# Performance work log

Measured on AMD Instinct MI355X. Metric: run time of the kernel, lower is better.

## Reference

```python
import jax, jax.numpy as jnp
import numpy as np

LEN_SORT_WINDOW = 2


def _butterfly_indices(v_len, d_v):
    # Column j is arange rolled right by s_j: s_0 = s_1 = 0, s_j = 2*(j-1) mod v_len.
    # (The butterfly_factor_to_matrix result in the original code is discarded;
    #  only the cyclic shifts matter.)
    shifts = np.zeros(d_v, dtype=np.int64)
    if d_v > 1:
        shifts[1:] = (LEN_SORT_WINDOW * np.arange(d_v - 1, dtype=np.int64)) % v_len
    rows = np.arange(v_len, dtype=np.int64)[:, None]
    return jnp.asarray((rows - shifts[None, :]) % v_len)  # [v_len, d_v] int64


def setup_inputs() -> dict:
    key = jax.random.key(0)
    B, L, D = 8, 4096, 1024
    v = jax.random.normal(key, (B, L, D), dtype=jnp.float32)
    return {"v": v}


def reference(v) -> jnp.ndarray:
    B, L, D = v.shape
    idx = _butterfly_indices(L, D)                       # [L, D]
    # gather: v_shifted[b,i,j] = v[b, idx[i,j], j]
    v_shifted = jnp.take_along_axis(v, jnp.broadcast_to(idx[None], (B, L, D)), axis=1)
    # windowed pairwise sort (ascending, window = 2) along the sequence dim
    pairs = v_shifted.reshape(B, L // LEN_SORT_WINDOW, LEN_SORT_WINDOW, D)
    v_sorted = jnp.sort(pairs, axis=2)
    return v_sorted.reshape(B, L, D)
```

## Files before the change

kernel.cpp:

```cpp
#include <hip/hip_runtime.h>

namespace {

constexpr int B  = 8;
constexpr int L  = 4096;
constexpr int D  = 1024;
constexpr int D4 = D / 4;
constexpr int P  = L / 2;
constexpr int TJ = 32;
constexpr int G  = TJ / 4;
constexpr int TP = 128;
constexpr int RTOT = TP + TJ;
constexpr int LDW  = TJ + 4;
constexpr int NT = 512;

__global__ __launch_bounds__(NT)
void swd_kernel(const float4* __restrict__ v, float4* __restrict__ out) {
  const int j0 = blockIdx.x * TJ;
  const int p0 = blockIdx.y * TP;
  const int b  = blockIdx.z;

  __shared__ __align__(16) float lds_m[RTOT][LDW];
  __shared__ __align__(16) float lds_M[RTOT][LDW];

  const int hmax = j0 + TJ - 2;
  const int r0   = p0 - hmax;

  const float4* __restrict__ vb = v + (size_t)b * L * D4 + (j0 >> 2);

  for (int idx = threadIdx.x; idx < RTOT * G; idx += NT) {
    const int k  = idx >> 3;
    const int fg = idx & 7;
    const int q  = (r0 + k) & (P - 1);
    const float4 a0 = vb[(size_t)(2 * q) * D4 + fg];
    const float4 a1 = vb[(size_t)(2 * q + 1) * D4 + fg];
    float4 m, M;
    m.x = fminf(a0.x, a1.x); M.x = fmaxf(a0.x, a1.x);
    m.y = fminf(a0.y, a1.y); M.y = fmaxf(a0.y, a1.y);
    m.z = fminf(a0.z, a1.z); M.z = fmaxf(a0.z, a1.z);
    m.w = fminf(a0.w, a1.w); M.w = fmaxf(a0.w, a1.w);
    *(float4*)&lds_m[k][4 * fg] = m;
    *(float4*)&lds_M[k][4 * fg] = M;
  }
  __syncthreads();

  const int g   = threadIdx.x & 7;
  const int c   = threadIdx.x >> 3;
  const int pp0 = c * 2;
  const int kx = pp0 + (TJ - 1) - 4 * g;

  const float4 m0 = *(const float4*)&lds_m[kx - 3][4 * g];
  const float4 m1 = *(const float4*)&lds_m[kx - 2][4 * g];
  const float4 m2 = *(const float4*)&lds_m[kx - 1][4 * g];
  const float4 m3 = *(const float4*)&lds_m[kx    ][4 * g];
  const float4 m4 = *(const float4*)&lds_m[kx + 1][4 * g];
  const float4 M0 = *(const float4*)&lds_M[kx - 3][4 * g];
  const float4 M1 = *(const float4*)&lds_M[kx - 2][4 * g];
  const float4 M2 = *(const float4*)&lds_M[kx - 1][4 * g];
  const float4 M3 = *(const float4*)&lds_M[kx    ][4 * g];
  const float4 M4 = *(const float4*)&lds_M[kx + 1][4 * g];

  const bool sp = (j0 == 0) && (g == 0);

  float4 e0, o0, e1, o1;
  e0.x = sp ? m2.x : m3.x; e0.y = m2.y; e0.z = m1.z; e0.w = m0.w;
  o0.x = sp ? M2.x : M3.x; o0.y = M2.y; o0.z = M1.z; o0.w = M0.w;
  e1.x = sp ? m3.x : m4.x; e1.y = m3.y; e1.z = m2.z; e1.w = m1.w;
  o1.x = sp ? M3.x : M4.x; o1.y = M3.y; o1.z = M2.z; o1.w = M1.w;

  float4* __restrict__ ob = out + (size_t)b * L * D4 + (j0 >> 2) + g;
  const size_t ro = (size_t)(2 * (p0 + pp0)) * D4;
  ob[ro]            = e0;
  ob[ro + D4]       = o0;
  ob[ro + 2 * D4]   = e1;
  ob[ro + 3 * D4]   = o1;
}

}

extern "C" void kernel_launch(void* const* d_in, const int* , int ,
                              void* d_out, int , void* , size_t ,
                              hipStream_t stream) {
  const float4* v = (const float4*)d_in[0];
  float4* out = (float4*)d_out;
  dim3 grid(D / TJ, P / TP, B);
  swd_kernel<<<grid, NT, 0, stream>>>(v, out);
}
```

Measured before the change: 235.8 us.

## Double-buffer async global-to-LDS loads across multiple pair tiles per block

Each block now handles four consecutive pair tiles of 64 instead of one tile of 128. Raw rows are loaded straight into a double-buffered LDS array with global_load_lds, and loading the next tile overlaps with computing the current one, using manual vmcnt waits and barriers. The min/max sort moves from the load phase to the read-from-LDS phase, and launch bounds request higher occupancy. In exchange, the halo overhead per tile grows because the tile is smaller, each pair is recomputed on read, and the hand-written waitcnt logic is fragile.

```diff
diff --git a/kernel.cpp b/kernel.cpp
--- a/kernel.cpp
+++ b/kernel.cpp
@@ -8,72 +8,99 @@
 constexpr int D4 = D / 4;
 constexpr int P  = L / 2;
 constexpr int TJ = 32;
-constexpr int G  = TJ / 4;
-constexpr int TP = 128;
-constexpr int RTOT = TP + TJ;
-constexpr int LDW  = TJ + 4;
+constexpr int TP = 64;
+constexpr int RP = TP + TJ;
+constexpr int RR = 2 * RP;
 constexpr int NT = 512;
+constexpr int NW = NT / 64;
+constexpr int T  = 4;
+constexpr int NCH = RR * TJ * 4 / 1024;
+constexpr int CPW = NCH / NW;
+static_assert(CPW == 3, "vmcnt literal below assumes 3 in-flight chunk loads");
+static_assert(2 * RR * TJ * 4 <= 49152, "LDS must stay well under 64 KiB");
 
-__global__ __launch_bounds__(NT)
-void swd_kernel(const float4* __restrict__ v, float4* __restrict__ out) {
+__device__ __forceinline__ void async_ld16(const float* g, float* l) {
+  __builtin_amdgcn_global_load_lds(
+      (const __attribute__((address_space(1))) void*)g,
+      (__attribute__((address_space(3))) void*)l, 16, 0, 0);
+}
+
+__global__ __launch_bounds__(NT, 6)
+void swd_kernel(const float* __restrict__ v, float4* __restrict__ out) {
   const int j0 = blockIdx.x * TJ;
-  const int p0 = blockIdx.y * TP;
+  const int ty = blockIdx.y;
   const int b  = blockIdx.z;
 
-  __shared__ __align__(16) float lds_m[RTOT][LDW];
-  __shared__ __align__(16) float lds_M[RTOT][LDW];
+  __shared__ float lds[2][RR * TJ];
 
-  const int hmax = j0 + TJ - 2;
-  const int r0   = p0 - hmax;
+  const int tid  = threadIdx.x;
+  const int wave = tid >> 6;
+  const int lane = tid & 63;
 
-  const float4* __restrict__ vb = v + (size_t)b * L * D4 + (j0 >> 2);
+  const float* __restrict__ vb = v + (size_t)b * L * D + j0;
 
-  for (int idx = threadIdx.x; idx < RTOT * G; idx += NT) {
-    const int k  = idx >> 3;
-    const int fg = idx & 7;
-    const int q  = (r0 + k) & (P - 1);
-    const float4 a0 = vb[(size_t)(2 * q) * D4 + fg];
-    const float4 a1 = vb[(size_t)(2 * q + 1) * D4 + fg];
-    float4 m, M;
-    m.x = fminf(a0.x, a1.x); M.x = fmaxf(a0.x, a1.x);
-    m.y = fminf(a0.y, a1.y); M.y = fmaxf(a0.y, a1.y);
-    m.z = fminf(a0.z, a1.z); M.z = fmaxf(a0.z, a1.z);
-    m.w = fminf(a0.w, a1.w); M.w = fmaxf(a0.w, a1.w);
-    *(float4*)&lds_m[k][4 * fg] = m;
-    *(float4*)&lds_M[k][4 * fg] = M;
-  }
-  __syncthreads();
+  const int f  = lane & 7;
+  const int kb = wave * 8 + (lane >> 3);
 
-  const int g   = threadIdx.x & 7;
-  const int c   = threadIdx.x >> 3;
-  const int pp0 = c * 2;
-  const int kx = pp0 + (TJ - 1) - 4 * g;
-
-  const float4 m0 = *(const float4*)&lds_m[kx - 3][4 * g];
-  const float4 m1 = *(const float4*)&lds_m[kx - 2][4 * g];
-  const float4 m2 = *(const float4*)&lds_m[kx - 1][4 * g];
-  const float4 m3 = *(const float4*)&lds_m[kx    ][4 * g];
-  const float4 m4 = *(const float4*)&lds_m[kx + 1][4 * g];
-  const float4 M0 = *(const float4*)&lds_M[kx - 3][4 * g];
-  const float4 M1 = *(const float4*)&lds_M[kx - 2][4 * g];
-  const float4 M2 = *(const float4*)&lds_M[kx - 1][4 * g];
-  const float4 M3 = *(const float4*)&lds_M[kx    ][4 * g];
-  const float4 M4 = *(const float4*)&lds_M[kx + 1][4 * g];
-
+  const int g   = tid & 7;
+  const int c   = tid >> 3;
+  const int krb = 2 * c - 8 * g + 2 * (TJ - 1) - 6;
   const bool sp = (j0 == 0) && (g == 0);
 
-  float4 e0, o0, e1, o1;
-  e0.x = sp ? m2.x : m3.x; e0.y = m2.y; e0.z = m1.z; e0.w = m0.w;
-  o0.x = sp ? M2.x : M3.x; o0.y = M2.y; o0.z = M1.z; o0.w = M0.w;
-  e1.x = sp ? m3.x : m4.x; e1.y = m3.y; e1.z = m2.z; e1.w = m1.w;
-  o1.x = sp ? M3.x : M4.x; o1.y = M3.y; o1.z = M2.z; o1.w = M1.w;
+  float4* __restrict__ ob = out + (size_t)b * L * D4 + (j0 >> 2) + g;
 
-  float4* __restrict__ ob = out + (size_t)b * L * D4 + (j0 >> 2) + g;
-  const size_t ro = (size_t)(2 * (p0 + pp0)) * D4;
-  ob[ro]            = e0;
-  ob[ro + D4]       = o0;
-  ob[ro + 2 * D4]   = e1;
-  ob[ro + 3 * D4]   = o1;
+  auto stage = [&](int tt, int s) {
+    const int p0 = tt * TP;
+    const int r0 = p0 - (j0 + TJ - 2);
+#pragma unroll
+    for (int i = 0; i < CPW; ++i) {
+      const int kr  = kb + 64 * i;
+      const int q   = (r0 + (kr >> 1)) & (P - 1);
+      const int row = 2 * q + (kr & 1);
+      async_ld16(vb + (size_t)row * D + 4 * f,
+                 &lds[s][(wave + NW * i) * (8 * TJ)]);
+    }
+  };
+
+  const int tt0 = ty * T;
+  stage(tt0, 0);
+
+#pragma unroll
+  for (int t = 0; t < T; ++t) {
+    if (t + 1 < T) {
+      stage(tt0 + t + 1, (t + 1) & 1);
+      asm volatile("s_waitcnt vmcnt(3)" ::: "memory");
+    } else {
+      asm volatile("s_waitcnt vmcnt(0)" ::: "memory");
+    }
+    __builtin_amdgcn_s_barrier();
+    asm volatile("" ::: "memory");
+
+    const float* Lb = lds[t & 1];
+
+    float4 m[4], M[4];
+#pragma unroll
+    for (int u = 0; u < 4; ++u) {
+      const float4 a0 = *(const float4*)&Lb[(krb + 2 * u)     * TJ + 4 * g];
+      const float4 a1 = *(const float4*)&Lb[(krb + 2 * u + 1) * TJ + 4 * g];
+      m[u].x = fminf(a0.x, a1.x); M[u].x = fmaxf(a0.x, a1.x);
+      m[u].y = fminf(a0.y, a1.y); M[u].y = fmaxf(a0.y, a1.y);
+      m[u].z = fminf(a0.z, a1.z); M[u].z = fmaxf(a0.z, a1.z);
+      m[u].w = fminf(a0.w, a1.w); M[u].w = fmaxf(a0.w, a1.w);
+    }
+
+    float4 e, o;
+    e.x = sp ? m[2].x : m[3].x; e.y = m[2].y; e.z = m[1].z; e.w = m[0].w;
+    o.x = sp ? M[2].x : M[3].x; o.y = M[2].y; o.z = M[1].z; o.w = M[0].w;
+
+    const size_t ro = (size_t)(2 * ((tt0 + t) * TP + c)) * D4;
+    ob[ro]      = e;
+    ob[ro + D4] = o;
+
+    asm volatile("s_waitcnt lgkmcnt(0)" ::: "memory");
+    __builtin_amdgcn_s_barrier();
+    asm volatile("" ::: "memory");
+  }
 }
 
 }
@@ -81,8 +108,8 @@
 extern "C" void kernel_launch(void* const* d_in, const int* , int ,
                               void* d_out, int , void* , size_t ,
                               hipStream_t stream) {
-  const float4* v = (const float4*)d_in[0];
+  const float* v = (const float*)d_in[0];
   float4* out = (float4*)d_out;
-  dim3 grid(D / TJ, P / TP, B);
+  dim3 grid(D / TJ, P / (T * TP), B);
   swd_kernel<<<grid, NT, 0, stream>>>(v, out);
 }
```

New measurement: 242.9 us. +3.0%, slower.
